# Kernel tuning notes

Measured on AMD Instinct MI355X. Metric: run time of the kernel, lower is better.

Reference implementation:

```python
import jax, jax.numpy as jnp
import numpy as np

N_NODES = 100000
N_EDGES = 1600000
IN_C = 128
DIM = 64
OUT_C = 64
BN_EPS = 1e-5


def _batchnorm(x, g, b):
    # training-mode BatchNorm1d: batch mean, biased variance
    m = jnp.mean(x, axis=0)
    v = jnp.var(x, axis=0)
    return (x - m) * jax.lax.rsqrt(v + BN_EPS) * g + b


def setup_inputs() -> dict:
    key = jax.random.key(0)
    ks = jax.random.split(key, 16)
    s = lambda fan: 1.0 / np.sqrt(fan)
    inp = {
        "X": jax.random.normal(ks[0], (N_NODES, IN_C), dtype=jnp.float32),
        "edge_index": jax.random.randint(ks[1], (2, N_EDGES), 0, N_NODES, dtype=jnp.int32),
        "edge_attr": jax.random.normal(ks[2], (N_EDGES, 1), dtype=jnp.float32),
        # bn_in over in_channels
        "bn_in_g": jnp.ones((IN_C,), jnp.float32),
        "bn_in_b": jnp.zeros((IN_C,), jnp.float32),
        # layer 0: edge lin 1->IN_C, node MLP IN_C->DIM
        "We0": jax.random.normal(ks[3], (1, IN_C), jnp.float32) * s(1),
        "be0": jnp.zeros((IN_C,), jnp.float32),
        "W0": jax.random.normal(ks[4], (IN_C, DIM), jnp.float32) * s(IN_C),
        "b0": jnp.zeros((DIM,), jnp.float32),
        "bn0_g": jnp.ones((DIM,), jnp.float32),
        "bn0_b": jnp.zeros((DIM,), jnp.float32),
        # layer 1: edge lin 1->DIM, node MLP DIM->DIM
        "We1": jax.random.normal(ks[5], (1, DIM), jnp.float32) * s(1),
        "be1": jnp.zeros((DIM,), jnp.float32),
        "W1": jax.random.normal(ks[6], (DIM, DIM), jnp.float32) * s(DIM),
        "b1": jnp.zeros((DIM,), jnp.float32),
        "bn1_g": jnp.ones((DIM,), jnp.float32),
        "bn1_b": jnp.zeros((DIM,), jnp.float32),
        # fc1: DIM->OUT_C, no bias
        "Wfc": jax.random.normal(ks[7], (DIM, OUT_C), jnp.float32) * s(DIM),
    }
    return inp


def reference(X, edge_index, edge_attr,
              bn_in_g, bn_in_b,
              We0, be0, W0, b0, bn0_g, bn0_b,
              We1, be1, W1, b1, bn1_g, bn1_b,
              Wfc):
    n = X.shape[0]
    src, dst = edge_index[0], edge_index[1]

    def gine(x, We, be, W, b):
        # GINEConv with eps=0: tanh(Linear(x + sum_j relu(x_j + lin(e_ij))))
        e = edge_attr @ We + be            # [E, C]
        msg = jax.nn.relu(x[src] + e)      # gather + edge-add + relu
        agg = jax.ops.segment_sum(msg, dst, num_segments=n)  # scatter-sum
        return jnp.tanh((x + agg) @ W + b)

    x = _batchnorm(X, bn_in_g, bn_in_b)
    h1 = _batchnorm(gine(x, We0, be0, W0, b0), bn0_g, bn0_b)
    h2 = _batchnorm(gine(h1, We1, be1, W1, b1), bn1_g, bn1_b)
    h3 = jnp.tanh(h2 @ Wfc)
    return jnp.concatenate([h1, h2, h3], axis=-1)  # [N, DIM+DIM+OUT_C]
```

## Files before the change

### kernel.cpp

```cpp
#include <hip/hip_runtime.h>
#include <hip/hip_fp16.h>
#include <math.h>
#include <stdint.h>

#define NN 100000
#define NE 1600000
#define INC 128
#define DIM 64
#define EPS 1e-5f
#define SB 512
#define NREP 8
#define NPART 8
#define PART_SZ ((NN + NPART - 1) / NPART)

struct __align__(8)  half4 { __half2 a, b; };
struct __align__(16) half8 { __half2 a, b, c, d; };

__device__ inline __half2 h2max(__half2 a, __half2 b) {
    __half2 r;
    asm("v_pk_max_f16 %0, %1, %2" : "=v"(r) : "v"(a), "v"(b));
    return r;
}

__global__ __launch_bounds__(256) void stats_hist_kernel(const float* __restrict__ X,
        const int* __restrict__ dst, int* __restrict__ counts,
        double* __restrict__ sum_out, double* __restrict__ sq_out) {
    __shared__ double ls[256], lq[256];
    if (blockIdx.x < SB) {
        int c  = threadIdx.x & 127;
        int rl = threadIdx.x >> 7;
        int row = blockIdx.x * 2 + rl;
        const int rstride = SB * 2;
        double s = 0.0, q = 0.0;
        for (int r = row; r < NN; r += rstride) {
            double v = (double)X[(size_t)r * INC + c];
            s += v; q += v * v;
        }
        ls[threadIdx.x] = s; lq[threadIdx.x] = q;
        __syncthreads();
        if (rl == 0) {
            s += ls[128 + c]; q += lq[128 + c];
            int rep = blockIdx.x & (NREP - 1);
            atomicAdd(&sum_out[rep * INC + c], s);
            atomicAdd(&sq_out[rep * INC + c], q);
        }
    } else {
        int bb = blockIdx.x - SB;
        int e = bb * 256 + threadIdx.x;
        if (e < NE) atomicAdd(&counts[(bb & (NREP - 1)) * NN + dst[e]], 1);
    }
}

template<int C>
__device__ inline void bn_fold_rep(int t, const double* dsum, const double* dsq,
                                   const float* g, const float* b, float* sc_s, float* sh_s) {
    if (t < C) {
        double s = 0.0, q = 0.0;
        #pragma unroll
        for (int r = 0; r < NREP; r++) { s += dsum[r * C + t]; q += dsq[r * C + t]; }
        double m = s / (double)NN;
        double v = q / (double)NN - m * m;
        double sc = (double)g[t] / sqrt(v + (double)EPS);
        sc_s[t] = (float)sc;
        sh_s[t] = (float)((double)b[t] - m * sc);
    }
}

__global__ __launch_bounds__(256) void xhat_half_kernel(const float* __restrict__ X,
        const double* __restrict__ dsum, const double* __restrict__ dsq,
        const float* __restrict__ g, const float* __restrict__ b,
        __half* __restrict__ Xh) {
    __shared__ float sc_s[INC], sh_s[INC];
    bn_fold_rep<INC>(threadIdx.x, dsum, dsq, g, b, sc_s, sh_s);
    __syncthreads();
    size_t i = (size_t)blockIdx.x * 256 + threadIdx.x;
    size_t e4 = i * 4;
    if (e4 >= (size_t)NN * INC) return;
    int c = (int)(e4 & 127);
    float4 x = *(const float4*)(X + e4);
    half4 h;
    h.a = __floats2half2_rn(fmaf(x.x, sc_s[c], sh_s[c]), fmaf(x.y, sc_s[c + 1], sh_s[c + 1]));
    h.b = __floats2half2_rn(fmaf(x.z, sc_s[c + 2], sh_s[c + 2]), fmaf(x.w, sc_s[c + 3], sh_s[c + 3]));
    *(half4*)(Xh + e4) = h;
}

__global__ __launch_bounds__(1024) void scan1_kernel(const int* __restrict__ counts,
                                                     int* __restrict__ offs, int* __restrict__ bsums) {
    __shared__ int tmp[2][1024];
    int t = threadIdx.x;
    int g = blockIdx.x * 1024 + t;
    int v = 0;
    if (g < NN) {
        #pragma unroll
        for (int r = 0; r < NREP; r++) v += counts[r * NN + g];
    }
    tmp[0][t] = v;
    __syncthreads();
    int pin = 0;
    for (int d = 1; d < 1024; d <<= 1) {
        int x = tmp[pin][t] + ((t >= d) ? tmp[pin][t - d] : 0);
        tmp[pin ^ 1][t] = x;
        pin ^= 1;
        __syncthreads();
    }
    int incl = tmp[pin][t];
    if (g < NN) offs[g] = incl - v;
    if (t == 1023) bsums[blockIdx.x] = incl;
}

__global__ __launch_bounds__(128) void scan2_kernel(int* __restrict__ bsums, int nb) {
    __shared__ int tmp[2][128];
    int t = threadIdx.x;
    int v = (t < nb) ? bsums[t] : 0;
    tmp[0][t] = v;
    __syncthreads();
    int pin = 0;
    for (int d = 1; d < 128; d <<= 1) {
        int x = tmp[pin][t] + ((t >= d) ? tmp[pin][t - d] : 0);
        tmp[pin ^ 1][t] = x;
        pin ^= 1;
        __syncthreads();
    }
    if (t < nb) bsums[t] = tmp[pin][t] - v;
}

__global__ __launch_bounds__(256) void scan3_kernel(int* __restrict__ offs, const int* __restrict__ bsums,
                                                    int* __restrict__ cursor) {
    int g = blockIdx.x * 256 + threadIdx.x;
    if (g < NN) {
        int o = offs[g] + bsums[g >> 10];
        offs[g] = o;
        cursor[g] = o;
    }
    if (g == 0) offs[NN] = NE;
}

__global__ __launch_bounds__(256) void scatter_kernel(const int* __restrict__ src, const int* __restrict__ dst,
                                                      const float* __restrict__ ea, int* __restrict__ cursor,
                                                      int2* __restrict__ src_ea) {
    const int p = blockIdx.x & (NPART - 1);
    const int blk = blockIdx.x >> 3;
    const int nblk = gridDim.x >> 3;
    const int lo = p * PART_SZ;
    const int hi = min(NN, lo + PART_SZ);
    for (int e = blk * 256 + threadIdx.x; e < NE; e += nblk * 256) {
        int d = dst[e];
        if (d >= lo && d < hi) {
            int pos = atomicAdd(&cursor[d], 1);
            src_ea[pos] = make_int2(src[e], __float_as_int(ea[e]));
        }
    }
}

__global__ __launch_bounds__(512, 8) void gine0_kernel(const float* __restrict__ X,
        const __half* __restrict__ Xh,
        const int* __restrict__ offs, const int2* __restrict__ src_ea,
        const double* __restrict__ dsum, const double* __restrict__ dsq,
        const float* __restrict__ g, const float* __restrict__ b,
        const float* __restrict__ We, const float* __restrict__ be,
        const float* __restrict__ W, const float* __restrict__ bvec,
        __half* __restrict__ t1h, double* __restrict__ dsum0, double* __restrict__ dsq0) {
    __shared__ __align__(16) float  u_s[32][INC + 4];
    __shared__ __align__(16) __half w_sh[DIM][INC + 8];
    __shared__ float sc_s[INC], sh_s[INC];
    const int t = threadIdx.x;
    const int row0 = blockIdx.x * 32;
    bn_fold_rep<INC>(t, dsum, dsq, g, b, sc_s, sh_s);
    for (int i = t; i < INC * DIM; i += 512) {
        int k = i >> 6, c = i & 63;
        w_sh[c][k] = __float2half_rn(W[i]);
    }
    __syncthreads();
    const int wid = t >> 6, l = t & 63;
    const int quarter = l >> 4;
    const int c8 = (l & 15) * 8;
    const __half2 z2 = __float2half2_rn(0.f);
    __half2 wvh0 = __floats2half2_rn(We[c8],     We[c8 + 1]);
    __half2 wvh1 = __floats2half2_rn(We[c8 + 2], We[c8 + 3]);
    __half2 wvh2 = __floats2half2_rn(We[c8 + 4], We[c8 + 5]);
    __half2 wvh3 = __floats2half2_rn(We[c8 + 6], We[c8 + 7]);
    __half2 bvh0 = __floats2half2_rn(be[c8],     be[c8 + 1]);
    __half2 bvh1 = __floats2half2_rn(be[c8 + 2], be[c8 + 3]);
    __half2 bvh2 = __floats2half2_rn(be[c8 + 4], be[c8 + 5]);
    __half2 bvh3 = __floats2half2_rn(be[c8 + 6], be[c8 + 7]);

    #define G0_ACC(vh, av2)  do { \
        ah0 = __hadd2(ah0, h2max(__hadd2((vh).a, __hfma2((av2), wvh0, bvh0)), z2)); \
        ah1 = __hadd2(ah1, h2max(__hadd2((vh).b, __hfma2((av2), wvh1, bvh1)), z2)); \
        ah2 = __hadd2(ah2, h2max(__hadd2((vh).c, __hfma2((av2), wvh2, bvh2)), z2)); \
        ah3 = __hadd2(ah3, h2max(__hadd2((vh).d, __hfma2((av2), wvh3, bvh3)), z2)); \
    } while (0)

    for (int nn = 0; nn < 4; ++nn) {
        int r = wid * 4 + nn;
        int n = row0 + r;
        __half2 ah0 = z2, ah1 = z2, ah2 = z2, ah3 = z2;
        if (n < NN) {
            int beg = offs[n], end = offs[n + 1];
            for (int base = beg; base < end; base += 64) {
                int j = base + l;
                int2 p = (j < end) ? src_ea[j] : make_int2(0, 0);
                float avf = __int_as_float(p.y);
                int cnt = min(64, end - base);
                int tt = 0;
                for (; tt + 8 <= cnt; tt += 8) {
                    int e0 = tt + quarter, e1 = tt + 4 + quarter;
                    int s0 = __shfl(p.x, e0), s1 = __shfl(p.x, e1);
                    float av0 = __shfl(avf, e0), av1 = __shfl(avf, e1);
                    half8 v0 = *(const half8*)(Xh + (size_t)s0 * INC + c8);
                    half8 v1 = *(const half8*)(Xh + (size_t)s1 * INC + c8);
                    __half2 a2_0 = __half2half2(__float2half_rn(av0));
                    __half2 a2_1 = __half2half2(__float2half_rn(av1));
                    G0_ACC(v0, a2_0); G0_ACC(v1, a2_1);
                }
                for (; tt < cnt; tt += 4) {
                    int e0 = tt + quarter;
                    int es = min(e0, cnt - 1);
                    int s0 = __shfl(p.x, es);
                    float av0 = __shfl(avf, es);
                    if (e0 < cnt) {
                        half8 v0 = *(const half8*)(Xh + (size_t)s0 * INC + c8);
                        __half2 a2_0 = __half2half2(__float2half_rn(av0));
                        G0_ACC(v0, a2_0);
                    }
                }
            }
        }
        float2 p0 = __half22float2(ah0), p1 = __half22float2(ah1);
        float2 p2 = __half22float2(ah2), p3 = __half22float2(ah3);
        float a0 = p0.x, a1 = p0.y, a2 = p1.x, a3 = p1.y;
        float a4 = p2.x, a5 = p2.y, a6 = p3.x, a7 = p3.y;
        a0 += __shfl_xor(a0, 16); a0 += __shfl_xor(a0, 32);
        a1 += __shfl_xor(a1, 16); a1 += __shfl_xor(a1, 32);
        a2 += __shfl_xor(a2, 16); a2 += __shfl_xor(a2, 32);
        a3 += __shfl_xor(a3, 16); a3 += __shfl_xor(a3, 32);
        a4 += __shfl_xor(a4, 16); a4 += __shfl_xor(a4, 32);
        a5 += __shfl_xor(a5, 16); a5 += __shfl_xor(a5, 32);
        a6 += __shfl_xor(a6, 16); a6 += __shfl_xor(a6, 32);
        a7 += __shfl_xor(a7, 16); a7 += __shfl_xor(a7, 32);
        if (quarter == 0) {
            if (n < NN) {
                float4 x0 = *(const float4*)(X + (size_t)n * INC + c8);
                float4 x1 = *(const float4*)(X + (size_t)n * INC + c8 + 4);
                a0 += fmaf(x0.x, sc_s[c8],     sh_s[c8]);
                a1 += fmaf(x0.y, sc_s[c8 + 1], sh_s[c8 + 1]);
                a2 += fmaf(x0.z, sc_s[c8 + 2], sh_s[c8 + 2]);
                a3 += fmaf(x0.w, sc_s[c8 + 3], sh_s[c8 + 3]);
                a4 += fmaf(x1.x, sc_s[c8 + 4], sh_s[c8 + 4]);
                a5 += fmaf(x1.y, sc_s[c8 + 5], sh_s[c8 + 5]);
                a6 += fmaf(x1.z, sc_s[c8 + 6], sh_s[c8 + 6]);
                a7 += fmaf(x1.w, sc_s[c8 + 7], sh_s[c8 + 7]);
            }
            *(float4*)&u_s[r][c8]     = make_float4(a0, a1, a2, a3);
            *(float4*)&u_s[r][c8 + 4] = make_float4(a4, a5, a6, a7);
        }
    }
    #undef G0_ACC
    __syncthreads();
    const int cc = t & 15;
    const int rg = t >> 4;
    float acc0 = bvec[cc], acc1 = bvec[cc + 16], acc2 = bvec[cc + 32], acc3 = bvec[cc + 48];
    #pragma unroll 2
    for (int k = 0; k < INC; k += 8) {
        float4 ua = *(const float4*)&u_s[rg][k];
        float4 ub = *(const float4*)&u_s[rg][k + 4];
        half8 w0 = *(const half8*)&w_sh[cc][k];
        half8 w1 = *(const half8*)&w_sh[cc + 16][k];
        half8 w2 = *(const half8*)&w_sh[cc + 32][k];
        half8 w3 = *(const half8*)&w_sh[cc + 48][k];
        float2 p;
        p = __half22float2(w0.a); acc0 = fmaf(ua.x, p.x, fmaf(ua.y, p.y, acc0));
        p = __half22float2(w0.b); acc0 = fmaf(ua.z, p.x, fmaf(ua.w, p.y, acc0));
        p = __half22float2(w0.c); acc0 = fmaf(ub.x, p.x, fmaf(ub.y, p.y, acc0));
        p = __half22float2(w0.d); acc0 = fmaf(ub.z, p.x, fmaf(ub.w, p.y, acc0));
        p = __half22float2(w1.a); acc1 = fmaf(ua.x, p.x, fmaf(ua.y, p.y, acc1));
        p = __half22float2(w1.b); acc1 = fmaf(ua.z, p.x, fmaf(ua.w, p.y, acc1));
        p = __half22float2(w1.c); acc1 = fmaf(ub.x, p.x, fmaf(ub.y, p.y, acc1));
        p = __half22float2(w1.d); acc1 = fmaf(ub.z, p.x, fmaf(ub.w, p.y, acc1));
        p = __half22float2(w2.a); acc2 = fmaf(ua.x, p.x, fmaf(ua.y, p.y, acc2));
        p = __half22float2(w2.b); acc2 = fmaf(ua.z, p.x, fmaf(ua.w, p.y, acc2));
        p = __half22float2(w2.c); acc2 = fmaf(ub.x, p.x, fmaf(ub.y, p.y, acc2));
        p = __half22float2(w2.d); acc2 = fmaf(ub.z, p.x, fmaf(ub.w, p.y, acc2));
        p = __half22float2(w3.a); acc3 = fmaf(ua.x, p.x, fmaf(ua.y, p.y, acc3));
        p = __half22float2(w3.b); acc3 = fmaf(ua.z, p.x, fmaf(ua.w, p.y, acc3));
        p = __half22float2(w3.c); acc3 = fmaf(ub.x, p.x, fmaf(ub.y, p.y, acc3));
        p = __half22float2(w3.d); acc3 = fmaf(ub.z, p.x, fmaf(ub.w, p.y, acc3));
    }
    int rr = row0 + rg;
    float t0 = tanhf(acc0), t1v = tanhf(acc1), t2v = tanhf(acc2), t3v = tanhf(acc3);
    if (rr < NN) {
        __half* op = t1h + (size_t)rr * DIM;
        op[cc]      = __float2half_rn(t0);
        op[cc + 16] = __float2half_rn(t1v);
        op[cc + 32] = __float2half_rn(t2v);
        op[cc + 48] = __float2half_rn(t3v);
    }
    __syncthreads();
    float* red_s = (float*)u_s;
    float* red_q = red_s + 2048;
    bool ok = (rr < NN);
    red_s[rg * 64 + cc]      = ok ? t0 : 0.f;
    red_s[rg * 64 + cc + 16] = ok ? t1v : 0.f;
    red_s[rg * 64 + cc + 32] = ok ? t2v : 0.f;
    red_s[rg * 64 + cc + 48] = ok ? t3v : 0.f;
    red_q[rg * 64 + cc]      = ok ? t0 * t0 : 0.f;
    red_q[rg * 64 + cc + 16] = ok ? t1v * t1v : 0.f;
    red_q[rg * 64 + cc + 32] = ok ? t2v * t2v : 0.f;
    red_q[rg * 64 + cc + 48] = ok ? t3v * t3v : 0.f;
    __syncthreads();
    if (t < 64) {
        float s = 0.f, q = 0.f;
        #pragma unroll
        for (int i = 0; i < 32; i++) { s += red_s[i * 64 + t]; q += red_q[i * 64 + t]; }
        int rep = blockIdx.x & (NREP - 1);
        atomicAdd(&dsum0[rep * DIM + t], (double)s);
        atomicAdd(&dsq0[rep * DIM + t], (double)q);
    }
}

__global__ __launch_bounds__(512) void gine1_kernel(const __half* __restrict__ t1h,
        const int* __restrict__ offs, const int2* __restrict__ src_ea,
        const double* __restrict__ dsum, const double* __restrict__ dsq,
        const float* __restrict__ g, const float* __restrict__ b,
        const float* __restrict__ We, const float* __restrict__ be,
        const float* __restrict__ W, const float* __restrict__ bvec,
        float* __restrict__ out, double* __restrict__ dsum1, double* __restrict__ dsq1) {
    __shared__ __align__(16) float u_s[64][DIM + 4];
    __shared__ __align__(16) float w_s[DIM][DIM + 4];
    __shared__ float sc_s[DIM], sh_s[DIM];
    const int t = threadIdx.x;
    const int row0 = blockIdx.x * 64;
    bn_fold_rep<DIM>(t, dsum, dsq, g, b, sc_s, sh_s);
    for (int i = t; i < DIM * DIM; i += 512) {
        int k = i >> 6, c = i & 63;
        w_s[c][k] = W[i];
    }
    __syncthreads();
    const int wid = t >> 6, l = t & 63;
    const int quarter = l >> 4;
    const int c4 = (l & 15) * 4;
    float4 wv = *(const float4*)(We + c4);
    float4 bv = *(const float4*)(be + c4);
    float4 sc4 = *(const float4*)(sc_s + c4);
    float4 sh4 = *(const float4*)(sh_s + c4);

    #define G1_ACC(vh, av)  do { \
        float2 f00 = __half22float2((vh).a), f01 = __half22float2((vh).b); \
        a0 += fmaxf(fmaf(f00.x, sc4.x, sh4.x) + fmaf((av), wv.x, bv.x), 0.f); \
        a1 += fmaxf(fmaf(f00.y, sc4.y, sh4.y) + fmaf((av), wv.y, bv.y), 0.f); \
        a2 += fmaxf(fmaf(f01.x, sc4.z, sh4.z) + fmaf((av), wv.z, bv.z), 0.f); \
        a3 += fmaxf(fmaf(f01.y, sc4.w, sh4.w) + fmaf((av), wv.w, bv.w), 0.f); \
    } while (0)

    for (int nn = 0; nn < 8; ++nn) {
        int r = wid * 8 + nn;
        int n = row0 + r;
        float a0 = 0.f, a1 = 0.f, a2 = 0.f, a3 = 0.f;
        if (n < NN) {
            int beg = offs[n], end = offs[n + 1];
            for (int base = beg; base < end; base += 64) {
                int j = base + l;
                int2 p = (j < end) ? src_ea[j] : make_int2(0, 0);
                float avf = __int_as_float(p.y);
                int cnt = min(64, end - base);
                int tt = 0;
                for (; tt + 8 <= cnt; tt += 8) {
                    int e0 = tt + quarter, e1 = tt + 4 + quarter;
                    int s0 = __shfl(p.x, e0), s1 = __shfl(p.x, e1);
                    float av0 = __shfl(avf, e0), av1 = __shfl(avf, e1);
                    half4 v0 = *(const half4*)(t1h + (size_t)s0 * DIM + c4);
                    half4 v1 = *(const half4*)(t1h + (size_t)s1 * DIM + c4);
                    G1_ACC(v0, av0); G1_ACC(v1, av1);
                }
                for (; tt < cnt; tt += 4) {
                    int e0 = tt + quarter;
                    int es = min(e0, cnt - 1);
                    int s0 = __shfl(p.x, es);
                    float av0 = __shfl(avf, es);
                    if (e0 < cnt) {
                        half4 v0 = *(const half4*)(t1h + (size_t)s0 * DIM + c4);
                        G1_ACC(v0, av0);
                    }
                }
            }
        }
        a0 += __shfl_xor(a0, 16); a0 += __shfl_xor(a0, 32);
        a1 += __shfl_xor(a1, 16); a1 += __shfl_xor(a1, 32);
        a2 += __shfl_xor(a2, 16); a2 += __shfl_xor(a2, 32);
        a3 += __shfl_xor(a3, 16); a3 += __shfl_xor(a3, 32);
        if (quarter == 0) {
            if (n < NN) {
                half4 h = *(const half4*)(t1h + (size_t)n * DIM + c4);
                float2 f0 = __half22float2(h.a), f1 = __half22float2(h.b);
                float h0 = fmaf(f0.x, sc4.x, sh4.x);
                float h1 = fmaf(f0.y, sc4.y, sh4.y);
                float h2 = fmaf(f1.x, sc4.z, sh4.z);
                float h3 = fmaf(f1.y, sc4.w, sh4.w);
                *(float4*)(out + (size_t)n * 192 + c4) = make_float4(h0, h1, h2, h3);
                a0 += h0; a1 += h1; a2 += h2; a3 += h3;
            }
            *(float4*)&u_s[r][c4] = make_float4(a0, a1, a2, a3);
        }
    }
    #undef G1_ACC
    __syncthreads();
    const int cc = t & 15;
    const int r0 = (t >> 4) * 2;
    float acc[2][4];
    #pragma unroll
    for (int j = 0; j < 4; j++) {
        float bj = bvec[cc + 16 * j];
        acc[0][j] = bj; acc[1][j] = bj;
    }
    #pragma unroll 4
    for (int k = 0; k < DIM; k += 4) {
        float4 w0 = *(const float4*)&w_s[cc][k];
        float4 w1 = *(const float4*)&w_s[cc + 16][k];
        float4 w2 = *(const float4*)&w_s[cc + 32][k];
        float4 w3 = *(const float4*)&w_s[cc + 48][k];
        #pragma unroll
        for (int i = 0; i < 2; i++) {
            float4 u = *(const float4*)&u_s[r0 + i][k];
            acc[i][0] = fmaf(u.x, w0.x, fmaf(u.y, w0.y, fmaf(u.z, w0.z, fmaf(u.w, w0.w, acc[i][0]))));
            acc[i][1] = fmaf(u.x, w1.x, fmaf(u.y, w1.y, fmaf(u.z, w1.z, fmaf(u.w, w1.w, acc[i][1]))));
            acc[i][2] = fmaf(u.x, w2.x, fmaf(u.y, w2.y, fmaf(u.z, w2.z, fmaf(u.w, w2.w, acc[i][2]))));
            acc[i][3] = fmaf(u.x, w3.x, fmaf(u.y, w3.y, fmaf(u.z, w3.z, fmaf(u.w, w3.w, acc[i][3]))));
        }
    }
    float tv[2][4];
    #pragma unroll
    for (int i = 0; i < 2; i++) {
        int rr = row0 + r0 + i;
        #pragma unroll
        for (int j = 0; j < 4; j++) tv[i][j] = tanhf(acc[i][j]);
        if (rr < NN) {
            float* op = out + (size_t)rr * 192 + 64;
            #pragma unroll
            for (int j = 0; j < 4; j++) op[cc + 16 * j] = tv[i][j];
        }
    }
    __syncthreads();
    float* red_s = (float*)w_s;
    float* red_q = red_s + 2048;
    const int rgp = t >> 4;
    bool ok0 = (row0 + r0 < NN), ok1 = (row0 + r0 + 1 < NN);
    #pragma unroll
    for (int j = 0; j < 4; j++) {
        float v0 = ok0 ? tv[0][j] : 0.f;
        float v1 = ok1 ? tv[1][j] : 0.f;
        red_s[rgp * 64 + cc + 16 * j] = v0 + v1;
        red_q[rgp * 64 + cc + 16 * j] = v0 * v0 + v1 * v1;
    }
    __syncthreads();
    if (t < 64) {
        float s = 0.f, q = 0.f;
        #pragma unroll
        for (int i = 0; i < 32; i++) { s += red_s[i * 64 + t]; q += red_q[i * 64 + t]; }
        int rep = blockIdx.x & (NREP - 1);
        atomicAdd(&dsum1[rep * DIM + t], (double)s);
        atomicAdd(&dsq1[rep * DIM + t], (double)q);
    }
}

__global__ __launch_bounds__(256) void fc_kernel(float* __restrict__ io,
        const double* __restrict__ dsum, const double* __restrict__ dsq,
        const float* __restrict__ g, const float* __restrict__ b,
        const float* __restrict__ W) {
    __shared__ __align__(16) float u_s[64][DIM + 4];
    __shared__ __align__(16) float w_s[DIM][DIM + 4];
    __shared__ float sc_s[DIM], sh_s[DIM];
    const int t = threadIdx.x;
    const int row0 = blockIdx.x * 64;
    bn_fold_rep<DIM>(t, dsum, dsq, g, b, sc_s, sh_s);
    __syncthreads();
    for (int i = t; i < DIM * DIM; i += 256) {
        int k = i >> 6, c = i & 63;
        w_s[c][k] = W[i];
    }
    for (int i = t; i < 64 * DIM; i += 256) {
        int r = i >> 6, k = i & 63;
        int rr = row0 + r;
        float v = 0.f;
        if (rr < NN) {
            size_t idx = (size_t)rr * 192 + 64 + k;
            v = fmaf(io[idx], sc_s[k], sh_s[k]);
            io[idx] = v;
        }
        u_s[r][k] = v;
    }
    __syncthreads();
    const int cc = t & 15;
    const int r0 = (t >> 4) << 2;
    float acc[4][4];
    #pragma unroll
    for (int j = 0; j < 4; j++) { acc[0][j] = 0.f; acc[1][j] = 0.f; acc[2][j] = 0.f; acc[3][j] = 0.f; }
    #pragma unroll 4
    for (int k = 0; k < DIM; k += 4) {
        float4 w0 = *(const float4*)&w_s[cc][k];
        float4 w1 = *(const float4*)&w_s[cc + 16][k];
        float4 w2 = *(const float4*)&w_s[cc + 32][k];
        float4 w3 = *(const float4*)&w_s[cc + 48][k];
        #pragma unroll
        for (int i = 0; i < 4; i++) {
            float4 u = *(const float4*)&u_s[r0 + i][k];
            acc[i][0] = fmaf(u.x, w0.x, fmaf(u.y, w0.y, fmaf(u.z, w0.z, fmaf(u.w, w0.w, acc[i][0]))));
            acc[i][1] = fmaf(u.x, w1.x, fmaf(u.y, w1.y, fmaf(u.z, w1.z, fmaf(u.w, w1.w, acc[i][1]))));
            acc[i][2] = fmaf(u.x, w2.x, fmaf(u.y, w2.y, fmaf(u.z, w2.z, fmaf(u.w, w2.w, acc[i][2]))));
            acc[i][3] = fmaf(u.x, w3.x, fmaf(u.y, w3.y, fmaf(u.z, w3.z, fmaf(u.w, w3.w, acc[i][3]))));
        }
    }
    #pragma unroll
    for (int i = 0; i < 4; i++) {
        int rr = row0 + r0 + i;
        if (rr < NN) {
            #pragma unroll
            for (int j = 0; j < 4; j++)
                io[(size_t)rr * 192 + 128 + cc + 16 * j] = tanhf(acc[i][j]);
        }
    }
}

extern "C" void kernel_launch(void* const* d_in, const int* in_sizes, int n_in,
                              void* d_out, int out_size, void* d_ws, size_t ws_size,
                              hipStream_t stream) {
    const float* X      = (const float*)d_in[0];
    const int*   ei     = (const int*)  d_in[1];
    const float* ea     = (const float*)d_in[2];
    const float* bng    = (const float*)d_in[3];
    const float* bnb    = (const float*)d_in[4];
    const float* We0    = (const float*)d_in[5];
    const float* be0    = (const float*)d_in[6];
    const float* W0     = (const float*)d_in[7];
    const float* b0     = (const float*)d_in[8];
    const float* bn0g   = (const float*)d_in[9];
    const float* bn0b   = (const float*)d_in[10];
    const float* We1    = (const float*)d_in[11];
    const float* be1    = (const float*)d_in[12];
    const float* W1     = (const float*)d_in[13];
    const float* b1     = (const float*)d_in[14];
    const float* bn1g   = (const float*)d_in[15];
    const float* bn1b   = (const float*)d_in[16];
    const float* Wfc    = (const float*)d_in[17];

    const int* src = ei;
    const int* dst = ei + NE;
    float* out = (float*)d_out;

    int2*   src_ea  = (int2*)d_ws;
    __half* t1h     = (__half*)(src_ea + NE);
    __half* Xh      = t1h + (size_t)NN * DIM;
    int*    counts  = (int*)(Xh + (size_t)NN * INC);
    int*    offs    = counts + (size_t)NREP * NN;
    int*    cursor  = offs + NN + 1;
    int*    bsums   = cursor + NN;
    double* dstats = (double*)(((uintptr_t)(bsums + 128) + 15) & ~(uintptr_t)15);
    double* dsum_in = dstats;
    double* dsq_in  = dsum_in + NREP * INC;
    double* dsum0   = dsq_in + NREP * INC;
    double* dsq0    = dsum0 + NREP * DIM;
    double* dsum1   = dsq0 + NREP * DIM;
    double* dsq1    = dsum1 + NREP * DIM;
    const size_t nstats = (size_t)NREP * (2 * INC + 4 * DIM);

    hipMemsetAsync(counts, 0, (size_t)NREP * NN * sizeof(int), stream);
    hipMemsetAsync(dstats, 0, nstats * sizeof(double), stream);

    stats_hist_kernel<<<SB + (NE + 255) / 256, 256, 0, stream>>>(X, dst, counts, dsum_in, dsq_in);

    xhat_half_kernel<<<(NN * INC / 4 + 255) / 256, 256, 0, stream>>>(X, dsum_in, dsq_in, bng, bnb, Xh);

    const int NB = (NN + 1023) / 1024;
    scan1_kernel<<<NB, 1024, 0, stream>>>(counts, offs, bsums);
    scan2_kernel<<<1, 128, 0, stream>>>(bsums, NB);
    scan3_kernel<<<(NN + 255) / 256, 256, 0, stream>>>(offs, bsums, cursor);
    scatter_kernel<<<2048, 256, 0, stream>>>(src, dst, ea, cursor, src_ea);

    gine0_kernel<<<(NN + 31) / 32, 512, 0, stream>>>(X, Xh, offs, src_ea, dsum_in, dsq_in, bng, bnb,
                                                     We0, be0, W0, b0, t1h, dsum0, dsq0);

    gine1_kernel<<<(NN + 63) / 64, 512, 0, stream>>>(t1h, offs, src_ea, dsum0, dsq0, bn0g, bn0b,
                                                     We1, be1, W1, b1, out, dsum1, dsq1);

    fc_kernel<<<(NN + 63) / 64, 256, 0, stream>>>(out, dsum1, dsq1, bn1g, bn1b, Wfc);
}
```

Before: 428.3 us.

## Precompute normalized h1 in half and accumulate gine1 messages in packed fp16

Adds a separate elementwise kernel that applies the layer-0 BatchNorm once per node, writes h1 to the output, and stores an fp16 copy that reuses the Xh buffer. gine1 then gathers the already-normalized fp16 rows and does the edge add, ReLU and sum with packed half2 arithmetic, removing the per-edge BN FMAs and the float conversions. The scatter partition count also drops from 8 to 4. The trade-offs are an extra kernel launch with an extra pass over memory, and lower precision, since neighbour sums now accumulate in fp16 with more rounding error.

```diff
diff --git a/kernel.cpp b/kernel.cpp
--- a/kernel.cpp
+++ b/kernel.cpp
@@ -10,7 +10,7 @@
 #define EPS 1e-5f
 #define SB 512
 #define NREP 8
-#define NPART 8
+#define NPART 4
 #define PART_SZ ((NN + NPART - 1) / NPART)
 
 struct __align__(8)  half4 { __half2 a, b; };
@@ -84,6 +84,31 @@
     *(half4*)(Xh + e4) = h;
 }
 
+__global__ __launch_bounds__(256) void h1_kernel(const __half* __restrict__ t1h,
+        const double* __restrict__ dsum, const double* __restrict__ dsq,
+        const float* __restrict__ g, const float* __restrict__ b,
+        float* __restrict__ out, __half* __restrict__ h1h) {
+    __shared__ float sc_s[DIM], sh_s[DIM];
+    bn_fold_rep<DIM>(threadIdx.x, dsum, dsq, g, b, sc_s, sh_s);
+    __syncthreads();
+    size_t i = (size_t)blockIdx.x * 256 + threadIdx.x;
+    size_t e4 = i * 4;
+    if (e4 >= (size_t)NN * DIM) return;
+    int c = (int)(e4 & 63);
+    size_t n = e4 >> 6;
+    half4 tv = *(const half4*)(t1h + e4);
+    float2 f0 = __half22float2(tv.a), f1 = __half22float2(tv.b);
+    float h0 = fmaf(f0.x, sc_s[c],     sh_s[c]);
+    float h1 = fmaf(f0.y, sc_s[c + 1], sh_s[c + 1]);
+    float h2 = fmaf(f1.x, sc_s[c + 2], sh_s[c + 2]);
+    float h3 = fmaf(f1.y, sc_s[c + 3], sh_s[c + 3]);
+    *(float4*)(out + n * 192 + c) = make_float4(h0, h1, h2, h3);
+    half4 hh;
+    hh.a = __floats2half2_rn(h0, h1);
+    hh.b = __floats2half2_rn(h2, h3);
+    *(half4*)(h1h + e4) = hh;
+}
+
 __global__ __launch_bounds__(1024) void scan1_kernel(const int* __restrict__ counts,
                                                      int* __restrict__ offs, int* __restrict__ bsums) {
     __shared__ int tmp[2][1024];
@@ -139,8 +164,8 @@
                                                       const float* __restrict__ ea, int* __restrict__ cursor,
                                                       int2* __restrict__ src_ea) {
     const int p = blockIdx.x & (NPART - 1);
-    const int blk = blockIdx.x >> 3;
-    const int nblk = gridDim.x >> 3;
+    const int blk = blockIdx.x >> 2;
+    const int nblk = gridDim.x >> 2;
     const int lo = p * PART_SZ;
     const int hi = min(NN, lo + PART_SZ);
     for (int e = blk * 256 + threadIdx.x; e < NE; e += nblk * 256) {
@@ -318,19 +343,15 @@
     }
 }
 
-__global__ __launch_bounds__(512) void gine1_kernel(const __half* __restrict__ t1h,
+__global__ __launch_bounds__(512) void gine1_kernel(const __half* __restrict__ h1h,
         const int* __restrict__ offs, const int2* __restrict__ src_ea,
-        const double* __restrict__ dsum, const double* __restrict__ dsq,
-        const float* __restrict__ g, const float* __restrict__ b,
         const float* __restrict__ We, const float* __restrict__ be,
         const float* __restrict__ W, const float* __restrict__ bvec,
         float* __restrict__ out, double* __restrict__ dsum1, double* __restrict__ dsq1) {
     __shared__ __align__(16) float u_s[64][DIM + 4];
     __shared__ __align__(16) float w_s[DIM][DIM + 4];
-    __shared__ float sc_s[DIM], sh_s[DIM];
     const int t = threadIdx.x;
     const int row0 = blockIdx.x * 64;
-    bn_fold_rep<DIM>(t, dsum, dsq, g, b, sc_s, sh_s);
     for (int i = t; i < DIM * DIM; i += 512) {
         int k = i >> 6, c = i & 63;
         w_s[c][k] = W[i];
@@ -339,23 +360,21 @@
     const int wid = t >> 6, l = t & 63;
     const int quarter = l >> 4;
     const int c4 = (l & 15) * 4;
-    float4 wv = *(const float4*)(We + c4);
-    float4 bv = *(const float4*)(be + c4);
-    float4 sc4 = *(const float4*)(sc_s + c4);
-    float4 sh4 = *(const float4*)(sh_s + c4);
-
-    #define G1_ACC(vh, av)  do { \
-        float2 f00 = __half22float2((vh).a), f01 = __half22float2((vh).b); \
-        a0 += fmaxf(fmaf(f00.x, sc4.x, sh4.x) + fmaf((av), wv.x, bv.x), 0.f); \
-        a1 += fmaxf(fmaf(f00.y, sc4.y, sh4.y) + fmaf((av), wv.y, bv.y), 0.f); \
-        a2 += fmaxf(fmaf(f01.x, sc4.z, sh4.z) + fmaf((av), wv.z, bv.z), 0.f); \
-        a3 += fmaxf(fmaf(f01.y, sc4.w, sh4.w) + fmaf((av), wv.w, bv.w), 0.f); \
+    const __half2 z2 = __float2half2_rn(0.f);
+    __half2 wvh0 = __floats2half2_rn(We[c4],     We[c4 + 1]);
+    __half2 wvh1 = __floats2half2_rn(We[c4 + 2], We[c4 + 3]);
+    __half2 bvh0 = __floats2half2_rn(be[c4],     be[c4 + 1]);
+    __half2 bvh1 = __floats2half2_rn(be[c4 + 2], be[c4 + 3]);
+
+    #define G1_ACC(vh, av2)  do { \
+        ah0 = __hadd2(ah0, h2max(__hadd2((vh).a, __hfma2((av2), wvh0, bvh0)), z2)); \
+        ah1 = __hadd2(ah1, h2max(__hadd2((vh).b, __hfma2((av2), wvh1, bvh1)), z2)); \
     } while (0)
 
     for (int nn = 0; nn < 8; ++nn) {
         int r = wid * 8 + nn;
         int n = row0 + r;
-        float a0 = 0.f, a1 = 0.f, a2 = 0.f, a3 = 0.f;
+        __half2 ah0 = z2, ah1 = z2;
         if (n < NN) {
             int beg = offs[n], end = offs[n + 1];
             for (int base = beg; base < end; base += 64) {
@@ -368,9 +387,11 @@
                     int e0 = tt + quarter, e1 = tt + 4 + quarter;
                     int s0 = __shfl(p.x, e0), s1 = __shfl(p.x, e1);
                     float av0 = __shfl(avf, e0), av1 = __shfl(avf, e1);
-                    half4 v0 = *(const half4*)(t1h + (size_t)s0 * DIM + c4);
-                    half4 v1 = *(const half4*)(t1h + (size_t)s1 * DIM + c4);
-                    G1_ACC(v0, av0); G1_ACC(v1, av1);
+                    half4 v0 = *(const half4*)(h1h + (size_t)s0 * DIM + c4);
+                    half4 v1 = *(const half4*)(h1h + (size_t)s1 * DIM + c4);
+                    __half2 a2_0 = __half2half2(__float2half_rn(av0));
+                    __half2 a2_1 = __half2half2(__float2half_rn(av1));
+                    G1_ACC(v0, a2_0); G1_ACC(v1, a2_1);
                 }
                 for (; tt < cnt; tt += 4) {
                     int e0 = tt + quarter;
@@ -378,26 +399,24 @@
                     int s0 = __shfl(p.x, es);
                     float av0 = __shfl(avf, es);
                     if (e0 < cnt) {
-                        half4 v0 = *(const half4*)(t1h + (size_t)s0 * DIM + c4);
-                        G1_ACC(v0, av0);
+                        half4 v0 = *(const half4*)(h1h + (size_t)s0 * DIM + c4);
+                        __half2 a2_0 = __half2half2(__float2half_rn(av0));
+                        G1_ACC(v0, a2_0);
                     }
                 }
             }
         }
+        float2 p0 = __half22float2(ah0), p1 = __half22float2(ah1);
+        float a0 = p0.x, a1 = p0.y, a2 = p1.x, a3 = p1.y;
         a0 += __shfl_xor(a0, 16); a0 += __shfl_xor(a0, 32);
         a1 += __shfl_xor(a1, 16); a1 += __shfl_xor(a1, 32);
         a2 += __shfl_xor(a2, 16); a2 += __shfl_xor(a2, 32);
         a3 += __shfl_xor(a3, 16); a3 += __shfl_xor(a3, 32);
         if (quarter == 0) {
             if (n < NN) {
-                half4 h = *(const half4*)(t1h + (size_t)n * DIM + c4);
+                half4 h = *(const half4*)(h1h + (size_t)n * DIM + c4);
                 float2 f0 = __half22float2(h.a), f1 = __half22float2(h.b);
-                float h0 = fmaf(f0.x, sc4.x, sh4.x);
-                float h1 = fmaf(f0.y, sc4.y, sh4.y);
-                float h2 = fmaf(f1.x, sc4.z, sh4.z);
-                float h3 = fmaf(f1.y, sc4.w, sh4.w);
-                *(float4*)(out + (size_t)n * 192 + c4) = make_float4(h0, h1, h2, h3);
-                a0 += h0; a1 += h1; a2 += h2; a3 += h3;
+                a0 += f0.x; a1 += f0.y; a2 += f1.x; a3 += f1.y;
             }
             *(float4*)&u_s[r][c4] = make_float4(a0, a1, a2, a3);
         }
@@ -549,6 +568,7 @@
     int2*   src_ea  = (int2*)d_ws;
     __half* t1h     = (__half*)(src_ea + NE);
     __half* Xh      = t1h + (size_t)NN * DIM;
+    __half* h1h     = Xh;
     int*    counts  = (int*)(Xh + (size_t)NN * INC);
     int*    offs    = counts + (size_t)NREP * NN;
     int*    cursor  = offs + NN + 1;
@@ -578,8 +598,10 @@
     gine0_kernel<<<(NN + 31) / 32, 512, 0, stream>>>(X, Xh, offs, src_ea, dsum_in, dsq_in, bng, bnb,
                                                      We0, be0, W0, b0, t1h, dsum0, dsq0);
 
-    gine1_kernel<<<(NN + 63) / 64, 512, 0, stream>>>(t1h, offs, src_ea, dsum0, dsq0, bn0g, bn0b,
-                                                     We1, be1, W1, b1, out, dsum1, dsq1);
+    h1_kernel<<<(NN * DIM / 4 + 255) / 256, 256, 0, stream>>>(t1h, dsum0, dsq0, bn0g, bn0b, out, h1h);
+
+    gine1_kernel<<<(NN + 63) / 64, 512, 0, stream>>>(h1h, offs, src_ea, We1, be1, W1, b1,
+                                                     out, dsum1, dsq1);
 
     fc_kernel<<<(NN + 63) / 64, 256, 0, stream>>>(out, dsum1, dsq1, bn1g, bn1b, Wfc);
 }
```

Result: faster. 418.8 us (-2.2%).
